# Optimization experiments

Hardware: AMD Instinct MI355X
Metric: run time of the kernel (lower is better)

Reference implementation:

```python
import jax, jax.numpy as jnp
import numpy as np

D_HEAD = 64  # module's self.heads scaling constant


def setup_inputs() -> dict:
    key = jax.random.key(0)
    kq, kk, kv = jax.random.split(key, 3)
    N, HW, C = 4, 4096, 64
    Q = jax.random.normal(kq, (N, HW, C), dtype=jnp.float32)
    K = jax.random.normal(kk, (N, HW, C), dtype=jnp.float32)
    V = jax.random.normal(kv, (N, HW, C), dtype=jnp.float32)
    return {"Q": Q, "K": K, "V": V}


def reference(Q, K, V):
    # logits[n, q, k] = Q[n,q,:] . K[n,k,:] / sqrt(d_head)
    scale = 1.0 / jnp.sqrt(jnp.asarray(D_HEAD, dtype=Q.dtype))
    logits = jnp.einsum("nqc,nkc->nqk", Q, K) * scale  # [N, HW, HW]
    # NOTE: softmax over the QUERY axis (dim=1), non-standard
    attn = jax.nn.softmax(logits, axis=1)
    return jnp.einsum("nqk,nkc->nqc", attn, V)
```

## Files before the change

### kernel.cpp

```cpp
#include <hip/hip_runtime.h>
#include <hip/hip_bf16.h>

#define NB 4
#define HWN 4096
#define CD 64
#define NSTRIDE (HWN * CD)

typedef short short8 __attribute__((ext_vector_type(8), may_alias));
typedef short short4v __attribute__((ext_vector_type(4), may_alias));
typedef float f32x4 __attribute__((ext_vector_type(4), may_alias));

__device__ constexpr float C1 = 0.18033688011112042f;

__device__ __forceinline__ unsigned short f2bf(float f) {
    unsigned u = __builtin_bit_cast(unsigned, f);
    u = (u + 0x7FFFu + ((u >> 16) & 1u)) >> 16;
    return (unsigned short)u;
}

__device__ __forceinline__ float fexp2(float x) {
#if __has_builtin(__builtin_amdgcn_exp2f)
    return __builtin_amdgcn_exp2f(x);
#else
    return exp2f(x);
#endif
}

__device__ __forceinline__ unsigned pk2(float a, float b) {
    __hip_bfloat162 h = __float22bfloat162_rn(float2{a, b});
    unsigned u;
    __builtin_memcpy(&u, &h, 4);
    return u;
}

__device__ __forceinline__ size_t qk_swz(int row, int c) {
    return (size_t)(row >> 4) * 1024 + (c >> 5) * 512 +
           ((((c >> 3) & 3) * 16 + (row & 15)) * 8) + (c & 7);
}

__global__ __launch_bounds__(256) void cvt_qk(const float* __restrict__ Q,
                                              const float* __restrict__ K,
                                              unsigned short* __restrict__ Qs,
                                              unsigned short* __restrict__ Ks,
                                              float* __restrict__ l) {
    if (blockIdx.x < 16) {
        int zi = blockIdx.x * 256 + threadIdx.x;
        *(f32x4*)(l + (size_t)zi * 4) = f32x4{0.f, 0.f, 0.f, 0.f};
    }
    int i = (blockIdx.x * 256 + threadIdx.x) * 4;
    int rg = i >> 6, c = i & 63;
    int n = rg >> 12, r = rg & 4095;
    float4 q = *(const float4*)(Q + i);
    float4 k = *(const float4*)(K + i);
    ushort4 qo, ko;
    qo.x = f2bf(q.x * C1); qo.y = f2bf(q.y * C1);
    qo.z = f2bf(q.z * C1); qo.w = f2bf(q.w * C1);
    ko.x = f2bf(k.x); ko.y = f2bf(k.y); ko.z = f2bf(k.z); ko.w = f2bf(k.w);
    size_t off = (size_t)n * NSTRIDE + qk_swz(r, c);
    *(ushort4*)(Qs + off) = qo;
    *(ushort4*)(Ks + off) = ko;
}

__global__ __attribute__((amdgpu_flat_work_group_size(256, 256), amdgpu_waves_per_eu(2, 4)))
void lsum_kernel(const unsigned short* __restrict__ Qs,
                 const unsigned short* __restrict__ Ks,
                 float* __restrict__ l) {
    int tid = threadIdx.x;
    int w = tid >> 6, lane = tid & 63, quad = lane >> 4, m16 = lane & 15;
    int n = blockIdx.y;
    int kbase = blockIdx.x * 256 + w * 64;

    const unsigned short* Kp = Ks + (size_t)n * NSTRIDE + (kbase >> 4) * 1024 + lane * 8;
    short8 ka0 = *(const short8*)(Kp);
    short8 ka1 = *(const short8*)(Kp + 512);
    short8 kb0 = *(const short8*)(Kp + 1024);
    short8 kb1 = *(const short8*)(Kp + 1536);
    short8 kc0 = *(const short8*)(Kp + 2048);
    short8 kc1 = *(const short8*)(Kp + 2560);
    short8 kd0 = *(const short8*)(Kp + 3072);
    short8 kd1 = *(const short8*)(Kp + 3584);

    const unsigned short* Qp = Qs + (size_t)n * NSTRIDE + blockIdx.z * 16384 + lane * 8;

    short8 qc0 = *(const short8*)(Qp);
    short8 qc1 = *(const short8*)(Qp + 512);
    Qp += 1024;

    float lA[4] = {0.f, 0.f, 0.f, 0.f};
    float lB[4] = {0.f, 0.f, 0.f, 0.f};
    float lC[4] = {0.f, 0.f, 0.f, 0.f};
    float lD[4] = {0.f, 0.f, 0.f, 0.f};
#pragma unroll 2
    for (int qc = 0; qc < 16; ++qc) {
        short8 qn0 = *(const short8*)(Qp);
        short8 qn1 = *(const short8*)(Qp + 512);
        f32x4 a = {0.f, 0.f, 0.f, 0.f}, b = a, c = a, d = a;
        __builtin_amdgcn_s_setprio(1);
        a = __builtin_amdgcn_mfma_f32_16x16x32_bf16(ka0, qc0, a, 0, 0, 0);
        a = __builtin_amdgcn_mfma_f32_16x16x32_bf16(ka1, qc1, a, 0, 0, 0);
        b = __builtin_amdgcn_mfma_f32_16x16x32_bf16(kb0, qc0, b, 0, 0, 0);
        b = __builtin_amdgcn_mfma_f32_16x16x32_bf16(kb1, qc1, b, 0, 0, 0);
        c = __builtin_amdgcn_mfma_f32_16x16x32_bf16(kc0, qc0, c, 0, 0, 0);
        c = __builtin_amdgcn_mfma_f32_16x16x32_bf16(kc1, qc1, c, 0, 0, 0);
        d = __builtin_amdgcn_mfma_f32_16x16x32_bf16(kd0, qc0, d, 0, 0, 0);
        d = __builtin_amdgcn_mfma_f32_16x16x32_bf16(kd1, qc1, d, 0, 0, 0);
        __builtin_amdgcn_s_setprio(0);
#pragma unroll
        for (int r = 0; r < 4; ++r) {
            lA[r] += fexp2(a[r]);
            lB[r] += fexp2(b[r]);
            lC[r] += fexp2(c[r]);
            lD[r] += fexp2(d[r]);
        }
        qc0 = qn0; qc1 = qn1;
        Qp += 1024;
    }
#pragma unroll
    for (int r = 0; r < 4; ++r)
        for (int d1 = 1; d1 < 16; d1 <<= 1) {
            lA[r] += __shfl_xor(lA[r], d1);
            lB[r] += __shfl_xor(lB[r], d1);
            lC[r] += __shfl_xor(lC[r], d1);
            lD[r] += __shfl_xor(lD[r], d1);
        }
    if (m16 == 0) {
        float* lp = l + n * HWN + kbase + quad * 4;
#pragma unroll
        for (int r = 0; r < 4; ++r) {
            atomicAdd(lp + r, lA[r]);
            atomicAdd(lp + 16 + r, lB[r]);
            atomicAdd(lp + 32 + r, lC[r]);
            atomicAdd(lp + 48 + r, lD[r]);
        }
    }
}

__global__ __launch_bounds__(256) void prep_v(const float* __restrict__ V,
                                              const float* __restrict__ l,
                                              unsigned short* __restrict__ Vts) {
    __shared__ float rl[64];
    __shared__ float tile[64][65];
    int tid = threadIdx.x, n = blockIdx.y, kbase = blockIdx.x * 64;
    if (tid < 64) rl[tid] = 1.0f / l[n * HWN + kbase + tid];
    __syncthreads();
#pragma unroll
    for (int i = 0; i < 16; ++i) {
        int e = i * 256 + tid;
        int k = e >> 6, c = e & 63;
        tile[c][k] = V[((size_t)(n * HWN + kbase + k)) * CD + c] * rl[k];
    }
    __syncthreads();
#pragma unroll
    for (int i = 0; i < 2; ++i) {
        int s = i * 256 + tid;
        int kb32 = s >> 8;
        int ct = (s >> 6) & 3;
        int ll = s & 63;
        int cc = ct * 16 + (ll & 15);
        int kq = ((ll >> 4) & 3) * 4;
        int k0 = kb32 * 32 + kq;
        short8 v;
#pragma unroll
        for (int j = 0; j < 4; ++j) {
            v[j]     = (short)f2bf(tile[cc][k0 + j]);
            v[4 + j] = (short)f2bf(tile[cc][k0 + 16 + j]);
        }
        size_t off = (size_t)n * NSTRIDE + (size_t)((kbase >> 5) + kb32) * 2048 +
                     ct * 512 + ll * 8;
        *(short8*)(Vts + off) = v;
    }
}

__global__ __attribute__((amdgpu_flat_work_group_size(256, 256), amdgpu_waves_per_eu(2, 4)))
void attn_kernel(const unsigned short* __restrict__ Qs,
                 const unsigned short* __restrict__ Ks,
                 const unsigned short* __restrict__ Vts,
                 float* __restrict__ partial,
                 int nit) {
    int tid = threadIdx.x;
    int w = tid >> 6, lane = tid & 63, quad = lane >> 4, m16 = lane & 15;
    int n = blockIdx.y;
    int qbase = blockIdx.x * 128 + w * 16;

    const unsigned short* Qp = Qs + (size_t)n * NSTRIDE + (qbase >> 4) * 1024 + lane * 8;
    short8 qa0 = *(const short8*)(Qp);
    short8 qa1 = *(const short8*)(Qp + 512);
    short8 qb0 = *(const short8*)(Qp + 4096);
    short8 qb1 = *(const short8*)(Qp + 4096 + 512);

    size_t kofs = (size_t)blockIdx.z * (size_t)nit * 2048;
    const unsigned short* Kp = Ks + (size_t)n * NSTRIDE + kofs + lane * 8;
    const unsigned short* Vp = Vts + (size_t)n * NSTRIDE + kofs + lane * 8;

    f32x4 oA[4], oB[4];
#pragma unroll
    for (int ct = 0; ct < 4; ++ct) { oA[ct] = f32x4{0.f, 0.f, 0.f, 0.f}; oB[ct] = oA[ct]; }

    short8 kf00 = *(const short8*)(Kp);
    short8 kf01 = *(const short8*)(Kp + 512);
    short8 kf10 = *(const short8*)(Kp + 1024);
    short8 kf11 = *(const short8*)(Kp + 1536);

#pragma unroll 2
    for (int it = 0; it < nit; ++it) {
        short8 kn00 = *(const short8*)(Kp + 2048);
        short8 kn01 = *(const short8*)(Kp + 2560);
        short8 kn10 = *(const short8*)(Kp + 3072);
        short8 kn11 = *(const short8*)(Kp + 3584);
        short8 vf0 = *(const short8*)(Vp);
        short8 vf1 = *(const short8*)(Vp + 512);
        short8 vf2 = *(const short8*)(Vp + 1024);
        short8 vf3 = *(const short8*)(Vp + 1536);

        f32x4 s00 = {0.f, 0.f, 0.f, 0.f}, s01 = s00, s10 = s00, s11 = s00;
        __builtin_amdgcn_s_setprio(1);
        s00 = __builtin_amdgcn_mfma_f32_16x16x32_bf16(kf00, qa0, s00, 0, 0, 0);
        s00 = __builtin_amdgcn_mfma_f32_16x16x32_bf16(kf01, qa1, s00, 0, 0, 0);
        s01 = __builtin_amdgcn_mfma_f32_16x16x32_bf16(kf10, qa0, s01, 0, 0, 0);
        s01 = __builtin_amdgcn_mfma_f32_16x16x32_bf16(kf11, qa1, s01, 0, 0, 0);
        s10 = __builtin_amdgcn_mfma_f32_16x16x32_bf16(kf00, qb0, s10, 0, 0, 0);
        s10 = __builtin_amdgcn_mfma_f32_16x16x32_bf16(kf01, qb1, s10, 0, 0, 0);
        s11 = __builtin_amdgcn_mfma_f32_16x16x32_bf16(kf10, qb0, s11, 0, 0, 0);
        s11 = __builtin_amdgcn_mfma_f32_16x16x32_bf16(kf11, qb1, s11, 0, 0, 0);
        __builtin_amdgcn_s_setprio(0);

        uint2 w00, w01, w10, w11;
        w00.x = pk2(fexp2(s00[0]), fexp2(s00[1])); w00.y = pk2(fexp2(s00[2]), fexp2(s00[3]));
        w01.x = pk2(fexp2(s01[0]), fexp2(s01[1])); w01.y = pk2(fexp2(s01[2]), fexp2(s01[3]));
        w10.x = pk2(fexp2(s10[0]), fexp2(s10[1])); w10.y = pk2(fexp2(s10[2]), fexp2(s10[3]));
        w11.x = pk2(fexp2(s11[0]), fexp2(s11[1])); w11.y = pk2(fexp2(s11[2]), fexp2(s11[3]));
        short4v pA0 = __builtin_bit_cast(short4v, w00);
        short4v pA1 = __builtin_bit_cast(short4v, w01);
        short4v pB0 = __builtin_bit_cast(short4v, w10);
        short4v pB1 = __builtin_bit_cast(short4v, w11);

        __builtin_amdgcn_s_setprio(1);
        {
            short4v vlo, vhi;
            vlo = __builtin_shufflevector(vf0, vf0, 0, 1, 2, 3);
            vhi = __builtin_shufflevector(vf0, vf0, 4, 5, 6, 7);
            oA[0] = __builtin_amdgcn_mfma_f32_16x16x16bf16_1k(vlo, pA0, oA[0], 0, 0, 0);
            oA[0] = __builtin_amdgcn_mfma_f32_16x16x16bf16_1k(vhi, pA1, oA[0], 0, 0, 0);
            oB[0] = __builtin_amdgcn_mfma_f32_16x16x16bf16_1k(vlo, pB0, oB[0], 0, 0, 0);
            oB[0] = __builtin_amdgcn_mfma_f32_16x16x16bf16_1k(vhi, pB1, oB[0], 0, 0, 0);
            vlo = __builtin_shufflevector(vf1, vf1, 0, 1, 2, 3);
            vhi = __builtin_shufflevector(vf1, vf1, 4, 5, 6, 7);
            oA[1] = __builtin_amdgcn_mfma_f32_16x16x16bf16_1k(vlo, pA0, oA[1], 0, 0, 0);
            oA[1] = __builtin_amdgcn_mfma_f32_16x16x16bf16_1k(vhi, pA1, oA[1], 0, 0, 0);
            oB[1] = __builtin_amdgcn_mfma_f32_16x16x16bf16_1k(vlo, pB0, oB[1], 0, 0, 0);
            oB[1] = __builtin_amdgcn_mfma_f32_16x16x16bf16_1k(vhi, pB1, oB[1], 0, 0, 0);
            vlo = __builtin_shufflevector(vf2, vf2, 0, 1, 2, 3);
            vhi = __builtin_shufflevector(vf2, vf2, 4, 5, 6, 7);
            oA[2] = __builtin_amdgcn_mfma_f32_16x16x16bf16_1k(vlo, pA0, oA[2], 0, 0, 0);
            oA[2] = __builtin_amdgcn_mfma_f32_16x16x16bf16_1k(vhi, pA1, oA[2], 0, 0, 0);
            oB[2] = __builtin_amdgcn_mfma_f32_16x16x16bf16_1k(vlo, pB0, oB[2], 0, 0, 0);
            oB[2] = __builtin_amdgcn_mfma_f32_16x16x16bf16_1k(vhi, pB1, oB[2], 0, 0, 0);
            vlo = __builtin_shufflevector(vf3, vf3, 0, 1, 2, 3);
            vhi = __builtin_shufflevector(vf3, vf3, 4, 5, 6, 7);
            oA[3] = __builtin_amdgcn_mfma_f32_16x16x16bf16_1k(vlo, pA0, oA[3], 0, 0, 0);
            oA[3] = __builtin_amdgcn_mfma_f32_16x16x16bf16_1k(vhi, pA1, oA[3], 0, 0, 0);
            oB[3] = __builtin_amdgcn_mfma_f32_16x16x16bf16_1k(vlo, pB0, oB[3], 0, 0, 0);
            oB[3] = __builtin_amdgcn_mfma_f32_16x16x16bf16_1k(vhi, pB1, oB[3], 0, 0, 0);
        }
        __builtin_amdgcn_s_setprio(0);

        kf00 = kn00; kf01 = kn01; kf10 = kn10; kf11 = kn11;
        Kp += 2048;
        Vp += 2048;
    }

    float* ppA = partial + (size_t)blockIdx.z * (NB * HWN * CD) +
                 ((size_t)(n * HWN + qbase + m16)) * CD + quad * 4;
    float* ppB = ppA + (size_t)64 * CD;
#pragma unroll
    for (int ct = 0; ct < 4; ++ct) {
        *(f32x4*)(ppA + ct * 16) = oA[ct];
        *(f32x4*)(ppB + ct * 16) = oB[ct];
    }
}

__global__ __launch_bounds__(256) void reduce_out(const float* __restrict__ p,
                                                  float* __restrict__ out, int ns) {
    int i = (blockIdx.x * 256 + threadIdx.x) * 4;
    f32x4 a = *(const f32x4*)(p + i);
    for (int s = 1; s < ns; ++s)
        a = a + *(const f32x4*)(p + (size_t)s * (NB * HWN * CD) + i);
    *(f32x4*)(out + i) = a;
}

extern "C" void kernel_launch(void* const* d_in, const int* in_sizes, int n_in,
                              void* d_out, int out_size, void* d_ws, size_t ws_size,
                              hipStream_t stream) {
    const float* Q = (const float*)d_in[0];
    const float* K = (const float*)d_in[1];
    const float* V = (const float*)d_in[2];
    float* out = (float*)d_out;

    char* ws = (char*)d_ws;
    unsigned short* Qs  = (unsigned short*)(ws);
    unsigned short* Ks  = (unsigned short*)(ws + (1u << 21));
    unsigned short* Vts = (unsigned short*)(ws + (2u << 21));
    float* l       = (float*)(ws + (3u << 21));
    float* partial = (float*)(ws + (4u << 21));

    size_t base = (size_t)(4u << 21);
    size_t slice = (size_t)NB * HWN * CD * sizeof(float);
    int ns = (ws_size >= base + 8 * slice) ? 8
           : (ws_size >= base + 4 * slice) ? 4 : 2;
    int nit = HWN / ns / 32;

    cvt_qk<<<1024, 256, 0, stream>>>(Q, K, Qs, Ks, l);
    lsum_kernel<<<dim3(16, NB, 16), 256, 0, stream>>>(Qs, Ks, l);
    prep_v<<<dim3(64, NB), 256, 0, stream>>>(V, l, Vts);
    attn_kernel<<<dim3(32, NB, ns), 256, 0, stream>>>(Qs, Ks, Vts, partial, nit);
    reduce_out<<<1024, 256, 0, stream>>>(partial, out, ns);
}
```

Measured before the change: 110.3 us.

## Permute K rows to use 16x16x32 MFMA for PV and fuse split reduction

```diff
diff --git a/kernel.cpp b/kernel.cpp
--- a/kernel.cpp
+++ b/kernel.cpp
@@ -9,6 +9,7 @@
 typedef short short8 __attribute__((ext_vector_type(8), may_alias));
 typedef short short4v __attribute__((ext_vector_type(4), may_alias));
 typedef float f32x4 __attribute__((ext_vector_type(4), may_alias));
+typedef unsigned int uint4v __attribute__((ext_vector_type(4), may_alias));
 
 __device__ constexpr float C1 = 0.18033688011112042f;
 
@@ -38,14 +39,23 @@
            ((((c >> 3) & 3) * 16 + (row & 15)) * 8) + (c & 7);
 }
 
+__device__ __forceinline__ int k_perm_row(int r) {
+    int G = r >> 5, a = r & 31;
+    int j = a & 7, g = a >> 3;
+    return (G << 5) + ((j >> 2) << 4) + g * 4 + (j & 3);
+}
+
 __global__ __launch_bounds__(256) void cvt_qk(const float* __restrict__ Q,
                                               const float* __restrict__ K,
                                               unsigned short* __restrict__ Qs,
                                               unsigned short* __restrict__ Ks,
-                                              float* __restrict__ l) {
+                                              float* __restrict__ l,
+                                              int* __restrict__ cnt) {
     if (blockIdx.x < 16) {
         int zi = blockIdx.x * 256 + threadIdx.x;
         *(f32x4*)(l + (size_t)zi * 4) = f32x4{0.f, 0.f, 0.f, 0.f};
+    } else if (blockIdx.x == 16 && threadIdx.x < NB * 32) {
+        cnt[threadIdx.x] = 0;
     }
     int i = (blockIdx.x * 256 + threadIdx.x) * 4;
     int rg = i >> 6, c = i & 63;
@@ -56,9 +66,8 @@
     qo.x = f2bf(q.x * C1); qo.y = f2bf(q.y * C1);
     qo.z = f2bf(q.z * C1); qo.w = f2bf(q.w * C1);
     ko.x = f2bf(k.x); ko.y = f2bf(k.y); ko.z = f2bf(k.z); ko.w = f2bf(k.w);
-    size_t off = (size_t)n * NSTRIDE + qk_swz(r, c);
-    *(ushort4*)(Qs + off) = qo;
-    *(ushort4*)(Ks + off) = ko;
+    *(ushort4*)(Qs + (size_t)n * NSTRIDE + qk_swz(r, c)) = qo;
+    *(ushort4*)(Ks + (size_t)n * NSTRIDE + qk_swz(k_perm_row(r), c)) = ko;
 }
 
 __global__ __attribute__((amdgpu_flat_work_group_size(256, 256), amdgpu_waves_per_eu(2, 4)))
@@ -124,13 +133,13 @@
             lD[r] += __shfl_xor(lD[r], d1);
         }
     if (m16 == 0) {
-        float* lp = l + n * HWN + kbase + quad * 4;
+        float* lp = l + n * HWN + kbase + quad * 8;
 #pragma unroll
         for (int r = 0; r < 4; ++r) {
             atomicAdd(lp + r, lA[r]);
-            atomicAdd(lp + 16 + r, lB[r]);
+            atomicAdd(lp + 4 + r, lB[r]);
             atomicAdd(lp + 32 + r, lC[r]);
-            atomicAdd(lp + 48 + r, lD[r]);
+            atomicAdd(lp + 36 + r, lD[r]);
         }
     }
 }
@@ -157,14 +166,11 @@
         int ct = (s >> 6) & 3;
         int ll = s & 63;
         int cc = ct * 16 + (ll & 15);
-        int kq = ((ll >> 4) & 3) * 4;
-        int k0 = kb32 * 32 + kq;
+        int k0 = kb32 * 32 + ((ll >> 4) & 3) * 8;
         short8 v;
 #pragma unroll
-        for (int j = 0; j < 4; ++j) {
-            v[j]     = (short)f2bf(tile[cc][k0 + j]);
-            v[4 + j] = (short)f2bf(tile[cc][k0 + 16 + j]);
-        }
+        for (int j = 0; j < 8; ++j)
+            v[j] = (short)f2bf(tile[cc][k0 + j]);
         size_t off = (size_t)n * NSTRIDE + (size_t)((kbase >> 5) + kb32) * 2048 +
                      ct * 512 + ll * 8;
         *(short8*)(Vts + off) = v;
@@ -176,7 +182,9 @@
                  const unsigned short* __restrict__ Ks,
                  const unsigned short* __restrict__ Vts,
                  float* __restrict__ partial,
-                 int nit) {
+                 float* __restrict__ out,
+                 int* __restrict__ cnt,
+                 int nit, int ns) {
     int tid = threadIdx.x;
     int w = tid >> 6, lane = tid & 63, quad = lane >> 4, m16 = lane & 15;
     int n = blockIdx.y;
@@ -224,44 +232,22 @@
         s11 = __builtin_amdgcn_mfma_f32_16x16x32_bf16(kf11, qb1, s11, 0, 0, 0);
         __builtin_amdgcn_s_setprio(0);
 
-        uint2 w00, w01, w10, w11;
-        w00.x = pk2(fexp2(s00[0]), fexp2(s00[1])); w00.y = pk2(fexp2(s00[2]), fexp2(s00[3]));
-        w01.x = pk2(fexp2(s01[0]), fexp2(s01[1])); w01.y = pk2(fexp2(s01[2]), fexp2(s01[3]));
-        w10.x = pk2(fexp2(s10[0]), fexp2(s10[1])); w10.y = pk2(fexp2(s10[2]), fexp2(s10[3]));
-        w11.x = pk2(fexp2(s11[0]), fexp2(s11[1])); w11.y = pk2(fexp2(s11[2]), fexp2(s11[3]));
-        short4v pA0 = __builtin_bit_cast(short4v, w00);
-        short4v pA1 = __builtin_bit_cast(short4v, w01);
-        short4v pB0 = __builtin_bit_cast(short4v, w10);
-        short4v pB1 = __builtin_bit_cast(short4v, w11);
+        uint4v wa = {pk2(fexp2(s00[0]), fexp2(s00[1])), pk2(fexp2(s00[2]), fexp2(s00[3])),
+                     pk2(fexp2(s01[0]), fexp2(s01[1])), pk2(fexp2(s01[2]), fexp2(s01[3]))};
+        uint4v wb = {pk2(fexp2(s10[0]), fexp2(s10[1])), pk2(fexp2(s10[2]), fexp2(s10[3])),
+                     pk2(fexp2(s11[0]), fexp2(s11[1])), pk2(fexp2(s11[2]), fexp2(s11[3]))};
+        short8 pA = __builtin_bit_cast(short8, wa);
+        short8 pB = __builtin_bit_cast(short8, wb);
 
         __builtin_amdgcn_s_setprio(1);
-        {
-            short4v vlo, vhi;
-            vlo = __builtin_shufflevector(vf0, vf0, 0, 1, 2, 3);
-            vhi = __builtin_shufflevector(vf0, vf0, 4, 5, 6, 7);
-            oA[0] = __builtin_amdgcn_mfma_f32_16x16x16bf16_1k(vlo, pA0, oA[0], 0, 0, 0);
-            oA[0] = __builtin_amdgcn_mfma_f32_16x16x16bf16_1k(vhi, pA1, oA[0], 0, 0, 0);
-            oB[0] = __builtin_amdgcn_mfma_f32_16x16x16bf16_1k(vlo, pB0, oB[0], 0, 0, 0);
-            oB[0] = __builtin_amdgcn_mfma_f32_16x16x16bf16_1k(vhi, pB1, oB[0], 0, 0, 0);
-            vlo = __builtin_shufflevector(vf1, vf1, 0, 1, 2, 3);
-            vhi = __builtin_shufflevector(vf1, vf1, 4, 5, 6, 7);
-            oA[1] = __builtin_amdgcn_mfma_f32_16x16x16bf16_1k(vlo, pA0, oA[1], 0, 0, 0);
-            oA[1] = __builtin_amdgcn_mfma_f32_16x16x16bf16_1k(vhi, pA1, oA[1], 0, 0, 0);
-            oB[1] = __builtin_amdgcn_mfma_f32_16x16x16bf16_1k(vlo, pB0, oB[1], 0, 0, 0);
-            oB[1] = __builtin_amdgcn_mfma_f32_16x16x16bf16_1k(vhi, pB1, oB[1], 0, 0, 0);
-            vlo = __builtin_shufflevector(vf2, vf2, 0, 1, 2, 3);
-            vhi = __builtin_shufflevector(vf2, vf2, 4, 5, 6, 7);
-            oA[2] = __builtin_amdgcn_mfma_f32_16x16x16bf16_1k(vlo, pA0, oA[2], 0, 0, 0);
-            oA[2] = __builtin_amdgcn_mfma_f32_16x16x16bf16_1k(vhi, pA1, oA[2], 0, 0, 0);
-            oB[2] = __builtin_amdgcn_mfma_f32_16x16x16bf16_1k(vlo, pB0, oB[2], 0, 0, 0);
-            oB[2] = __builtin_amdgcn_mfma_f32_16x16x16bf16_1k(vhi, pB1, oB[2], 0, 0, 0);
-            vlo = __builtin_shufflevector(vf3, vf3, 0, 1, 2, 3);
-            vhi = __builtin_shufflevector(vf3, vf3, 4, 5, 6, 7);
-            oA[3] = __builtin_amdgcn_mfma_f32_16x16x16bf16_1k(vlo, pA0, oA[3], 0, 0, 0);
-            oA[3] = __builtin_amdgcn_mfma_f32_16x16x16bf16_1k(vhi, pA1, oA[3], 0, 0, 0);
-            oB[3] = __builtin_amdgcn_mfma_f32_16x16x16bf16_1k(vlo, pB0, oB[3], 0, 0, 0);
-            oB[3] = __builtin_amdgcn_mfma_f32_16x16x16bf16_1k(vhi, pB1, oB[3], 0, 0, 0);
-        }
+        oA[0] = __builtin_amdgcn_mfma_f32_16x16x32_bf16(vf0, pA, oA[0], 0, 0, 0);
+        oB[0] = __builtin_amdgcn_mfma_f32_16x16x32_bf16(vf0, pB, oB[0], 0, 0, 0);
+        oA[1] = __builtin_amdgcn_mfma_f32_16x16x32_bf16(vf1, pA, oA[1], 0, 0, 0);
+        oB[1] = __builtin_amdgcn_mfma_f32_16x16x32_bf16(vf1, pB, oB[1], 0, 0, 0);
+        oA[2] = __builtin_amdgcn_mfma_f32_16x16x32_bf16(vf2, pA, oA[2], 0, 0, 0);
+        oB[2] = __builtin_amdgcn_mfma_f32_16x16x32_bf16(vf2, pB, oB[2], 0, 0, 0);
+        oA[3] = __builtin_amdgcn_mfma_f32_16x16x32_bf16(vf3, pA, oA[3], 0, 0, 0);
+        oB[3] = __builtin_amdgcn_mfma_f32_16x16x32_bf16(vf3, pB, oB[3], 0, 0, 0);
         __builtin_amdgcn_s_setprio(0);
 
         kf00 = kn00; kf01 = kn01; kf10 = kn10; kf11 = kn11;
@@ -277,15 +263,26 @@
         *(f32x4*)(ppA + ct * 16) = oA[ct];
         *(f32x4*)(ppB + ct * 16) = oB[ct];
     }
-}
-
-__global__ __launch_bounds__(256) void reduce_out(const float* __restrict__ p,
-                                                  float* __restrict__ out, int ns) {
-    int i = (blockIdx.x * 256 + threadIdx.x) * 4;
-    f32x4 a = *(const f32x4*)(p + i);
-    for (int s = 1; s < ns; ++s)
-        a = a + *(const f32x4*)(p + (size_t)s * (NB * HWN * CD) + i);
-    *(f32x4*)(out + i) = a;
+
+    __threadfence();
+    __syncthreads();
+    __shared__ int sdone;
+    if (tid == 0) {
+        int old = atomicAdd(cnt + n * 32 + blockIdx.x, 1);
+        sdone = (old == ns - 1);
+    }
+    __syncthreads();
+    if (sdone) {
+        __threadfence();
+        size_t qb = ((size_t)n * HWN + (size_t)blockIdx.x * 128) * CD;
+        for (int i = tid; i < 2048; i += 256) {
+            const float* pp = partial + qb + (size_t)i * 4;
+            f32x4 a = *(const f32x4*)(pp);
+            for (int s = 1; s < ns; ++s)
+                a = a + *(const f32x4*)(pp + (size_t)s * (NB * HWN * CD));
+            *(f32x4*)(out + qb + (size_t)i * 4) = a;
+        }
+    }
 }
 
 extern "C" void kernel_launch(void* const* d_in, const int* in_sizes, int n_in,
@@ -301,6 +298,7 @@
     unsigned short* Ks  = (unsigned short*)(ws + (1u << 21));
     unsigned short* Vts = (unsigned short*)(ws + (2u << 21));
     float* l       = (float*)(ws + (3u << 21));
+    int*   cnt     = (int*)(ws + (3u << 21) + 65536);
     float* partial = (float*)(ws + (4u << 21));
 
     size_t base = (size_t)(4u << 21);
@@ -309,9 +307,8 @@
            : (ws_size >= base + 4 * slice) ? 4 : 2;
     int nit = HWN / ns / 32;
 
-    cvt_qk<<<1024, 256, 0, stream>>>(Q, K, Qs, Ks, l);
+    cvt_qk<<<1024, 256, 0, stream>>>(Q, K, Qs, Ks, l, cnt);
     lsum_kernel<<<dim3(16, NB, 16), 256, 0, stream>>>(Qs, Ks, l);
     prep_v<<<dim3(64, NB), 256, 0, stream>>>(V, l, Vts);
-    attn_kernel<<<dim3(32, NB, ns), 256, 0, stream>>>(Qs, Ks, Vts, partial, nit);
-    reduce_out<<<1024, 256, 0, stream>>>(partial, out, ns);
-}
+    attn_kernel<<<dim3(32, NB, ns), 256, 0, stream>>>(Qs, Ks, Vts, partial, out, cnt, nit, ns);
+}
```

New measurement: 270.5 us. +145.3%, slower.
